# Optimization experiments

Measured on AMD Instinct MI355X. Metric: run time of the kernel, lower is better.

Reference implementation:

```python
import jax, jax.numpy as jnp
import numpy as np

BATCH_SIZE = 4096
DIM = 128
TEMPERATURE = 0.5
EPS = 1e-8


def setup_inputs() -> dict:
    key = jax.random.key(0)
    k1, k2 = jax.random.split(key)
    z_i = jax.random.normal(k1, (BATCH_SIZE, DIM), dtype=jnp.float32)
    z_j = jax.random.normal(k2, (BATCH_SIZE, DIM), dtype=jnp.float32)
    return {"z_i": z_i, "z_j": z_j}


def reference(z_i, z_j):
    B = z_i.shape[0]
    N = 2 * B
    z = jnp.concatenate([z_i, z_j], axis=0)  # [N, D]
    # cosine similarity = matmul of L2-normalized rows (avoids the NxNxD broadcast)
    zn = z / jnp.maximum(jnp.linalg.norm(z, axis=1, keepdims=True), EPS)
    sim = (zn @ zn.T) / TEMPERATURE  # [N, N]
    idx = jnp.arange(N)
    # positive pair: row i pairs with row (i+B) mod N (covers both diag offsets +B and -B)
    pos = sim[idx, (idx + B) % N]  # [N]
    # CE over logits [pos, negatives]; the logit set per row is the full sim row
    # minus the self-similarity (diagonal). Mask diagonal with a large negative.
    neg_inf = jnp.asarray(-1e9, sim.dtype)
    sim_masked = jnp.where(idx[:, None] == idx[None, :], neg_inf, sim)
    lse = jax.nn.logsumexp(sim_masked, axis=1)  # [N]
    # CrossEntropyLoss(reduction='sum') with label 0 (the positive), divided by N
    loss = jnp.sum(lse - pos) / N
    return loss
```

## Files before the change

### kernel.cpp

```cpp
#include <hip/hip_runtime.h>
#include <cstdint>


#define BROWS 4096
#define NROWS 8192
#define ROWB  256
#define CSPL  24
#define CTILES 512
#define BRT   256
#define TILEB 4096

typedef __attribute__((ext_vector_type(8))) __bf16    bf16x8;
typedef __attribute__((ext_vector_type(4))) float     f32x4;
typedef __attribute__((ext_vector_type(4))) uint32_t  u32x4;

#define K1F 2.8853900817779268f
#define LN2F 0.69314718055994531f
#define BC8(x) __builtin_bit_cast(bf16x8, x)

__device__ __forceinline__ uint16_t f2bf(float f) {
    uint32_t u = __builtin_bit_cast(uint32_t, f);
    u = (u + 0x7FFFu + ((u >> 16) & 1u)) >> 16;
    return (uint16_t)u;
}
__device__ __forceinline__ float bf2f(uint16_t b) {
    return __builtin_bit_cast(float, ((uint32_t)b) << 16);
}
__device__ __forceinline__ void gload_lds16(const void* g, void* l) {
    __builtin_amdgcn_global_load_lds(
        (const __attribute__((address_space(1))) void*)g,
        (__attribute__((address_space(3))) void*)l, 16, 0, 0);
}

__global__ __launch_bounds__(256) void k_normalize(
    const float* __restrict__ zi, const float* __restrict__ zj,
    uint16_t* __restrict__ znA, uint16_t* __restrict__ znB)
{
    int tid  = threadIdx.x;
    int lane = tid & 63;
    int wid  = tid >> 6;
    int li   = lane & 7;
    int row  = blockIdx.x * 32 + wid * 8 + (lane >> 3);

    const float* src = (row < BROWS) ? (zi + (size_t)row * 128)
                                     : (zj + (size_t)(row - BROWS) * 128);
    float4 v[4];
    const float4* s4 = (const float4*)(src + li * 16);
#pragma unroll
    for (int c = 0; c < 4; ++c) v[c] = s4[c];

    float ss = 0.f;
#pragma unroll
    for (int c = 0; c < 4; ++c)
        ss += v[c].x*v[c].x + v[c].y*v[c].y + v[c].z*v[c].z + v[c].w*v[c].w;
#pragma unroll
    for (int off = 1; off < 8; off <<= 1) ss += __shfl_xor(ss, off);

    float scale = 1.0f / fmaxf(sqrtf(ss), 1e-8f);

    float e[16];
#pragma unroll
    for (int c = 0; c < 4; ++c) {
        e[c*4+0] = v[c].x * scale; e[c*4+1] = v[c].y * scale;
        e[c*4+2] = v[c].z * scale; e[c*4+3] = v[c].w * scale;
    }
    uint32_t wB[8], wA[8];
#pragma unroll
    for (int q = 0; q < 8; ++q) {
        wB[q] = (uint32_t)f2bf(e[2*q])       | ((uint32_t)f2bf(e[2*q+1])       << 16);
        wA[q] = (uint32_t)f2bf(e[2*q] * K1F) | ((uint32_t)f2bf(e[2*q+1] * K1F) << 16);
    }
    uint4* dB = (uint4*)((char*)znB + (size_t)row * ROWB + li * 32);
    dB[0] = make_uint4(wB[0], wB[1], wB[2], wB[3]);
    dB[1] = make_uint4(wB[4], wB[5], wB[6], wB[7]);
    uint4* dA = (uint4*)((char*)znA + (size_t)row * ROWB + li * 32);
    dA[0] = make_uint4(wA[0], wA[1], wA[2], wA[3]);
    dA[1] = make_uint4(wA[4], wA[5], wA[6], wA[7]);
}

__global__ __launch_bounds__(256)
__attribute__((amdgpu_waves_per_eu(3, 3)))
void k_simlse(
    const uint16_t* __restrict__ znA, const uint16_t* __restrict__ znB,
    float* __restrict__ partial)
{
    __shared__ __align__(16) char lds[2][TILEB];

    const char* zA = (const char*)znA;
    const char* zB = (const char*)znB;
    int tid  = threadIdx.x;
    int lane = tid & 63;
    int wid  = tid >> 6;
    int lo16 = lane & 15;
    int hi4  = lane >> 4;
    int rowBase = blockIdx.x * BRT + wid * 64;

    u32x4 a[4][4];
#pragma unroll
    for (int rt = 0; rt < 4; ++rt) {
        const char* ap = zA + (size_t)(rowBase + rt * 16 + lo16) * ROWB + hi4 * 16;
#pragma unroll
        for (int kf = 0; kf < 4; ++kf)
            a[rt][kf] = *(const u32x4*)(ap + kf * 64);
    }

    float rs[4][4];
#pragma unroll
    for (int rt = 0; rt < 4; ++rt)
#pragma unroll
        for (int r = 0; r < 4; ++r) rs[rt][r] = 0.f;

    int t0 = (CTILES * blockIdx.y) / CSPL;
    int t1 = (CTILES * (blockIdx.y + 1)) / CSPL;
    int nt = t1 - t0;

    const char* gsrc = zB + (size_t)t0 * TILEB
                     + ((tid * 16) ^ (((tid >> 4) & 7) << 4));
    char* ldst[2] = { &lds[0][wid * 1024], &lds[1][wid * 1024] };
    int  xorv = (lo16 & 7) << 4;

#define STAGE(sel, t) gload_lds16(gsrc + (size_t)(t) * TILEB, ldst[sel])

#define COMPUTE(sel) do {                                                        \
        const char* lb_ = &lds[sel][lo16 * 256];                                 \
        u32x4 bf[4];                                                             \
        _Pragma("unroll")                                                        \
        for (int kf = 0; kf < 4; ++kf)                                           \
            bf[kf] = *(const u32x4*)(lb_ + ((hi4 * 16 + kf * 64) ^ xorv));       \
        f32x4 ac0 = {0.f,0.f,0.f,0.f}, ac1 = {0.f,0.f,0.f,0.f};                  \
        f32x4 ac2 = {0.f,0.f,0.f,0.f}, ac3 = {0.f,0.f,0.f,0.f};                  \
        _Pragma("unroll")                                                        \
        for (int kf = 0; kf < 4; ++kf) {                                         \
            bf16x8 bk_ = BC8(bf[kf]);                                            \
            ac0 = __builtin_amdgcn_mfma_f32_16x16x32_bf16(BC8(a[0][kf]), bk_, ac0, 0, 0, 0); \
            ac1 = __builtin_amdgcn_mfma_f32_16x16x32_bf16(BC8(a[1][kf]), bk_, ac1, 0, 0, 0); \
            ac2 = __builtin_amdgcn_mfma_f32_16x16x32_bf16(BC8(a[2][kf]), bk_, ac2, 0, 0, 0); \
            ac3 = __builtin_amdgcn_mfma_f32_16x16x32_bf16(BC8(a[3][kf]), bk_, ac3, 0, 0, 0); \
        }                                                                        \
        _Pragma("unroll")                                                        \
        for (int r = 0; r < 4; ++r) {                                            \
            rs[0][r] += __builtin_amdgcn_exp2f(ac0[r]);                          \
            rs[1][r] += __builtin_amdgcn_exp2f(ac1[r]);                          \
            rs[2][r] += __builtin_amdgcn_exp2f(ac2[r]);                          \
            rs[3][r] += __builtin_amdgcn_exp2f(ac3[r]);                          \
        }                                                                        \
    } while (0)

    STAGE(0, 0);
    __syncthreads();

    for (int t = 0; t < nt; ++t) {
        if (t + 1 < nt) STAGE((t + 1) & 1, t + 1);
        COMPUTE(t & 1);
        __syncthreads();
    }

#undef STAGE
#undef COMPUTE

#pragma unroll
    for (int rt = 0; rt < 4; ++rt)
#pragma unroll
        for (int r = 0; r < 4; ++r) {
            float s = rs[rt][r];
            s += __shfl_xor(s, 1);  s += __shfl_xor(s, 2);
            s += __shfl_xor(s, 4);  s += __shfl_xor(s, 8);
            if (lo16 == 0) {
                int row = rowBase + rt * 16 + hi4 * 4 + r;
                partial[blockIdx.y * NROWS + row] = s;
            }
        }
}

__global__ __launch_bounds__(256) void k_finalize(
    const uint16_t* __restrict__ znA, const uint16_t* __restrict__ znB,
    const float* __restrict__ partial, float* __restrict__ blocksum)
{
    int tid = threadIdx.x;
    int i = blockIdx.x * 256 + tid;

    float S = 0.f;
#pragma unroll
    for (int cs = 0; cs < CSPL; ++cs) S += partial[cs * NROWS + i];

    int j = (i + BROWS) & (NROWS - 1);
    const uint4* rAi = (const uint4*)((const char*)znA + (size_t)i * ROWB);
    const uint4* rBi = (const uint4*)((const char*)znB + (size_t)i * ROWB);
    const uint4* rBj = (const uint4*)((const char*)znB + (size_t)j * ROWB);
    float adot = 0.f;
    float sdot = 0.f;
#pragma unroll
    for (int c = 0; c < 16; ++c) {
        uint4 ua = rAi[c], ub = rBi[c], vb = rBj[c];
        const uint32_t* pa = (const uint32_t*)&ua;
        const uint32_t* pb = (const uint32_t*)&ub;
        const uint32_t* pv = (const uint32_t*)&vb;
#pragma unroll
        for (int q = 0; q < 4; ++q) {
            float a0 = bf2f((uint16_t)(pa[q] & 0xffffu)), a1 = bf2f((uint16_t)(pa[q] >> 16));
            float b0 = bf2f((uint16_t)(pb[q] & 0xffffu)), b1 = bf2f((uint16_t)(pb[q] >> 16));
            float v0 = bf2f((uint16_t)(pv[q] & 0xffffu)), v1 = bf2f((uint16_t)(pv[q] >> 16));
            adot += a0 * v0 + a1 * v1;
            sdot += a0 * b0 + a1 * b1;
        }
    }
    S -= __builtin_amdgcn_exp2f(sdot);
    float c = LN2F * (__builtin_amdgcn_logf(S) - adot);

#pragma unroll
    for (int off = 1; off < 64; off <<= 1) c += __shfl_xor(c, off);
    __shared__ float wsum[4];
    int lane = tid & 63, wid = tid >> 6;
    if (lane == 0) wsum[wid] = c;
    __syncthreads();
    if (tid == 0) blocksum[blockIdx.x] = wsum[0] + wsum[1] + wsum[2] + wsum[3];
}

__global__ __launch_bounds__(64) void k_reduce(
    const float* __restrict__ blocksum, float* __restrict__ out)
{
    int tid = threadIdx.x;
    float v = (tid < 32) ? blocksum[tid] : 0.f;
#pragma unroll
    for (int off = 1; off < 64; off <<= 1) v += __shfl_xor(v, off);
    if (tid == 0) out[0] = v * (1.0f / (float)NROWS);
}

extern "C" void kernel_launch(void* const* d_in, const int* in_sizes, int n_in,
                              void* d_out, int out_size, void* d_ws, size_t ws_size,
                              hipStream_t stream)
{
    const float* zi = (const float*)d_in[0];
    const float* zj = (const float*)d_in[1];
    float* out = (float*)d_out;

    char* ws = (char*)d_ws;
    uint16_t* znA      = (uint16_t*)ws;
    uint16_t* znB      = (uint16_t*)(ws + (size_t)NROWS * ROWB);
    float*    partial  = (float*)(ws + 2 * (size_t)NROWS * ROWB);
    float*    blocksum = (float*)(ws + 2 * (size_t)NROWS * ROWB
                                     + (size_t)CSPL * NROWS * 4);

    k_normalize<<<dim3(256), dim3(256), 0, stream>>>(zi, zj, znA, znB);
    k_simlse  <<<dim3(32, CSPL), dim3(256), 0, stream>>>(znA, znB, partial);
    k_finalize<<<dim3(32), dim3(256), 0, stream>>>(znA, znB, partial, blocksum);
    k_reduce  <<<dim3(1), dim3(64), 0, stream>>>(blocksum, out);
}
```

Measured before the change: 41.62 us.

## Triple-buffer 32-column B tiles with prefetch depth two and one barrier

The column tile is doubled to 32 rows of B per stage and the LDS ring grows to three buffers. Loads are now issued two tiles ahead, and explicit vmcnt waits replace the per-iteration __syncthreads, leaving a single s_barrier per tile. The aim is to hide global-to-LDS latency better and to halve the number of loop iterations and barriers. In exchange the block uses three times the LDS (24 KB), which could limit occupancy, and correctness now depends on the hand-written waitcnt counts.

```diff
diff --git a/kernel.cpp b/kernel.cpp
--- a/kernel.cpp
+++ b/kernel.cpp
@@ -6,9 +6,9 @@
 #define NROWS 8192
 #define ROWB  256
 #define CSPL  24
-#define CTILES 512
+#define CT32  256
 #define BRT   256
-#define TILEB 4096
+#define TILEB 8192
 
 typedef __attribute__((ext_vector_type(8))) __bf16    bf16x8;
 typedef __attribute__((ext_vector_type(4))) float     f32x4;
@@ -84,7 +84,7 @@
     const uint16_t* __restrict__ znA, const uint16_t* __restrict__ znB,
     float* __restrict__ partial)
 {
-    __shared__ __align__(16) char lds[2][TILEB];
+    __shared__ __align__(16) char lds[3][TILEB];
 
     const char* zA = (const char*)znA;
     const char* zB = (const char*)znB;
@@ -110,50 +110,63 @@
 #pragma unroll
         for (int r = 0; r < 4; ++r) rs[rt][r] = 0.f;
 
-    int t0 = (CTILES * blockIdx.y) / CSPL;
-    int t1 = (CTILES * (blockIdx.y + 1)) / CSPL;
+    int t0 = (CT32 * blockIdx.y) / CSPL;
+    int t1 = (CT32 * (blockIdx.y + 1)) / CSPL;
     int nt = t1 - t0;
 
     const char* gsrc = zB + (size_t)t0 * TILEB
                      + ((tid * 16) ^ (((tid >> 4) & 7) << 4));
-    char* ldst[2] = { &lds[0][wid * 1024], &lds[1][wid * 1024] };
-    int  xorv = (lo16 & 7) << 4;
-
-#define STAGE(sel, t) gload_lds16(gsrc + (size_t)(t) * TILEB, ldst[sel])
+    int xorv = (lo16 & 7) << 4;
+
+#define STAGE(sel, t) do {                                                     \
+        const char* g_ = gsrc + (size_t)(t) * TILEB;                           \
+        gload_lds16(g_,        &lds[sel][wid * 1024]);                         \
+        gload_lds16(g_ + 4096, &lds[sel][4096 + wid * 1024]);                  \
+    } while (0)
 
 #define COMPUTE(sel) do {                                                        \
-        const char* lb_ = &lds[sel][lo16 * 256];                                 \
-        u32x4 bf[4];                                                             \
         _Pragma("unroll")                                                        \
-        for (int kf = 0; kf < 4; ++kf)                                           \
-            bf[kf] = *(const u32x4*)(lb_ + ((hi4 * 16 + kf * 64) ^ xorv));       \
-        f32x4 ac0 = {0.f,0.f,0.f,0.f}, ac1 = {0.f,0.f,0.f,0.f};                  \
-        f32x4 ac2 = {0.f,0.f,0.f,0.f}, ac3 = {0.f,0.f,0.f,0.f};                  \
-        _Pragma("unroll")                                                        \
-        for (int kf = 0; kf < 4; ++kf) {                                         \
-            bf16x8 bk_ = BC8(bf[kf]);                                            \
-            ac0 = __builtin_amdgcn_mfma_f32_16x16x32_bf16(BC8(a[0][kf]), bk_, ac0, 0, 0, 0); \
-            ac1 = __builtin_amdgcn_mfma_f32_16x16x32_bf16(BC8(a[1][kf]), bk_, ac1, 0, 0, 0); \
-            ac2 = __builtin_amdgcn_mfma_f32_16x16x32_bf16(BC8(a[2][kf]), bk_, ac2, 0, 0, 0); \
-            ac3 = __builtin_amdgcn_mfma_f32_16x16x32_bf16(BC8(a[3][kf]), bk_, ac3, 0, 0, 0); \
-        }                                                                        \
-        _Pragma("unroll")                                                        \
-        for (int r = 0; r < 4; ++r) {                                            \
-            rs[0][r] += __builtin_amdgcn_exp2f(ac0[r]);                          \
-            rs[1][r] += __builtin_amdgcn_exp2f(ac1[r]);                          \
-            rs[2][r] += __builtin_amdgcn_exp2f(ac2[r]);                          \
-            rs[3][r] += __builtin_amdgcn_exp2f(ac3[r]);                          \
+        for (int ct = 0; ct < 2; ++ct) {                                         \
+            const char* lb_ = &lds[sel][ct * 4096 + lo16 * 256];                 \
+            u32x4 bf[4];                                                         \
+            _Pragma("unroll")                                                    \
+            for (int kf = 0; kf < 4; ++kf)                                       \
+                bf[kf] = *(const u32x4*)(lb_ + ((hi4 * 16 + kf * 64) ^ xorv));   \
+            f32x4 ac0 = {0.f,0.f,0.f,0.f}, ac1 = {0.f,0.f,0.f,0.f};              \
+            f32x4 ac2 = {0.f,0.f,0.f,0.f}, ac3 = {0.f,0.f,0.f,0.f};              \
+            _Pragma("unroll")                                                    \
+            for (int kf = 0; kf < 4; ++kf) {                                     \
+                bf16x8 bk_ = BC8(bf[kf]);                                        \
+                ac0 = __builtin_amdgcn_mfma_f32_16x16x32_bf16(BC8(a[0][kf]), bk_, ac0, 0, 0, 0); \
+                ac1 = __builtin_amdgcn_mfma_f32_16x16x32_bf16(BC8(a[1][kf]), bk_, ac1, 0, 0, 0); \
+                ac2 = __builtin_amdgcn_mfma_f32_16x16x32_bf16(BC8(a[2][kf]), bk_, ac2, 0, 0, 0); \
+                ac3 = __builtin_amdgcn_mfma_f32_16x16x32_bf16(BC8(a[3][kf]), bk_, ac3, 0, 0, 0); \
+            }                                                                    \
+            _Pragma("unroll")                                                    \
+            for (int r = 0; r < 4; ++r) {                                        \
+                rs[0][r] += __builtin_amdgcn_exp2f(ac0[r]);                      \
+                rs[1][r] += __builtin_amdgcn_exp2f(ac1[r]);                      \
+                rs[2][r] += __builtin_amdgcn_exp2f(ac2[r]);                      \
+                rs[3][r] += __builtin_amdgcn_exp2f(ac3[r]);                      \
+            }                                                                    \
         }                                                                        \
     } while (0)
 
     STAGE(0, 0);
-    __syncthreads();
-
-    for (int t = 0; t < nt; ++t) {
-        if (t + 1 < nt) STAGE((t + 1) & 1, t + 1);
-        COMPUTE(t & 1);
-        __syncthreads();
-    }
+    STAGE(1, 1);
+
+    int t = 0;
+    for (; t < nt - 1; ++t) {
+        asm volatile("s_waitcnt vmcnt(2)" ::: "memory");
+        __builtin_amdgcn_s_barrier();
+        __builtin_amdgcn_sched_barrier(0);
+        COMPUTE(t % 3);
+        if (t + 2 < nt) STAGE((t + 2) % 3, t + 2);
+    }
+    asm volatile("s_waitcnt vmcnt(0)" ::: "memory");
+    __builtin_amdgcn_s_barrier();
+    __builtin_amdgcn_sched_barrier(0);
+    COMPUTE(t % 3);
 
 #undef STAGE
 #undef COMPUTE
```

Result: faster. 39.09 us (-6.1%).

## Exploit similarity-matrix symmetry by computing only upper-triangular block tiles

Applied to the files above, without the earlier changes.

The similarity kernel now launches one block per half of each upper-triangular 256x256 block pair, using a triangular index mapping. Each tile's exp values feed both the row sums and column sums, and the column sums are written as extra partial slots for the mirrored rows. This roughly halves the MFMA and exp work. It also replaces the double-buffered loop with a fully unrolled four-stage prefetch that uses explicit vmcnt waits. In exchange, finalize reads a variable number of partial slots per row, the workspace for partials grows, and the kernel uses more LDS plus an extra cross-wave column reduction.

```diff
diff --git a/kernel.cpp b/kernel.cpp
--- a/kernel.cpp
+++ b/kernel.cpp
@@ -5,10 +5,8 @@
 #define BROWS 4096
 #define NROWS 8192
 #define ROWB  256
-#define CSPL  24
-#define CTILES 512
-#define BRT   256
-#define TILEB 4096
+#define TILEB 8192
+#define NSLOT 96
 
 typedef __attribute__((ext_vector_type(8))) __bf16    bf16x8;
 typedef __attribute__((ext_vector_type(4))) float     f32x4;
@@ -84,7 +82,8 @@
     const uint16_t* __restrict__ znA, const uint16_t* __restrict__ znB,
     float* __restrict__ partial)
 {
-    __shared__ __align__(16) char lds[2][TILEB];
+    __shared__ __align__(16) char lds[4][TILEB];
+    __shared__ float cslds[4 * 128];
 
     const char* zA = (const char*)znA;
     const char* zB = (const char*)znB;
@@ -93,7 +92,15 @@
     int wid  = tid >> 6;
     int lo16 = lane & 15;
     int hi4  = lane >> 4;
-    int rowBase = blockIdx.x * BRT + wid * 64;
+
+    int q = blockIdx.x;
+    int p = q >> 1, h = q & 1;
+    int s = p / 33, w = p % 33;
+    int bx, by;
+    if (w < 32 - s) { by = s;      bx = s + w; }
+    else            { by = 31 - s; bx = by + (w - (32 - s)); }
+
+    int rowBase = bx * 256 + wid * 64;
 
     u32x4 a[4][4];
 #pragma unroll
@@ -109,67 +116,100 @@
     for (int rt = 0; rt < 4; ++rt)
 #pragma unroll
         for (int r = 0; r < 4; ++r) rs[rt][r] = 0.f;
-
-    int t0 = (CTILES * blockIdx.y) / CSPL;
-    int t1 = (CTILES * (blockIdx.y + 1)) / CSPL;
-    int nt = t1 - t0;
-
-    const char* gsrc = zB + (size_t)t0 * TILEB
+    float cs[8];
+#pragma unroll
+    for (int tg = 0; tg < 8; ++tg) cs[tg] = 0.f;
+
+    const char* gsrc = zB + (size_t)(by * 8 + h * 4) * TILEB
                      + ((tid * 16) ^ (((tid >> 4) & 7) << 4));
-    char* ldst[2] = { &lds[0][wid * 1024], &lds[1][wid * 1024] };
-    int  xorv = (lo16 & 7) << 4;
-
-#define STAGE(sel, t) gload_lds16(gsrc + (size_t)(t) * TILEB, ldst[sel])
-
-#define COMPUTE(sel) do {                                                        \
-        const char* lb_ = &lds[sel][lo16 * 256];                                 \
-        u32x4 bf[4];                                                             \
-        _Pragma("unroll")                                                        \
-        for (int kf = 0; kf < 4; ++kf)                                           \
-            bf[kf] = *(const u32x4*)(lb_ + ((hi4 * 16 + kf * 64) ^ xorv));       \
-        f32x4 ac0 = {0.f,0.f,0.f,0.f}, ac1 = {0.f,0.f,0.f,0.f};                  \
-        f32x4 ac2 = {0.f,0.f,0.f,0.f}, ac3 = {0.f,0.f,0.f,0.f};                  \
-        _Pragma("unroll")                                                        \
-        for (int kf = 0; kf < 4; ++kf) {                                         \
-            bf16x8 bk_ = BC8(bf[kf]);                                            \
-            ac0 = __builtin_amdgcn_mfma_f32_16x16x32_bf16(BC8(a[0][kf]), bk_, ac0, 0, 0, 0); \
-            ac1 = __builtin_amdgcn_mfma_f32_16x16x32_bf16(BC8(a[1][kf]), bk_, ac1, 0, 0, 0); \
-            ac2 = __builtin_amdgcn_mfma_f32_16x16x32_bf16(BC8(a[2][kf]), bk_, ac2, 0, 0, 0); \
-            ac3 = __builtin_amdgcn_mfma_f32_16x16x32_bf16(BC8(a[3][kf]), bk_, ac3, 0, 0, 0); \
-        }                                                                        \
-        _Pragma("unroll")                                                        \
-        for (int r = 0; r < 4; ++r) {                                            \
-            rs[0][r] += __builtin_amdgcn_exp2f(ac0[r]);                          \
-            rs[1][r] += __builtin_amdgcn_exp2f(ac1[r]);                          \
-            rs[2][r] += __builtin_amdgcn_exp2f(ac2[r]);                          \
-            rs[3][r] += __builtin_amdgcn_exp2f(ac3[r]);                          \
-        }                                                                        \
+    int xorv = (lo16 & 7) << 4;
+
+#define STAGE(sel) do {                                                        \
+        const char* g_ = gsrc + (size_t)(sel) * TILEB;                         \
+        gload_lds16(g_,        &lds[sel][wid * 1024]);                         \
+        gload_lds16(g_ + 4096, &lds[sel][4096 + wid * 1024]);                  \
     } while (0)
 
-    STAGE(0, 0);
-    __syncthreads();
-
-    for (int t = 0; t < nt; ++t) {
-        if (t + 1 < nt) STAGE((t + 1) & 1, t + 1);
-        COMPUTE(t & 1);
-        __syncthreads();
-    }
+#define SUBTILE(sel, ct, TG) do {                                              \
+        const char* lb_ = &lds[sel][(ct) * 4096 + lo16 * 256];                 \
+        u32x4 bf0 = *(const u32x4*)(lb_ + ((hi4 * 16 +   0) ^ xorv));          \
+        u32x4 bf1 = *(const u32x4*)(lb_ + ((hi4 * 16 +  64) ^ xorv));          \
+        u32x4 bf2 = *(const u32x4*)(lb_ + ((hi4 * 16 + 128) ^ xorv));          \
+        u32x4 bf3 = *(const u32x4*)(lb_ + ((hi4 * 16 + 192) ^ xorv));          \
+        f32x4 A0 = {0.f,0.f,0.f,0.f}, A1 = {0.f,0.f,0.f,0.f};                  \
+        f32x4 A2 = {0.f,0.f,0.f,0.f}, A3 = {0.f,0.f,0.f,0.f};                  \
+        A0 = __builtin_amdgcn_mfma_f32_16x16x32_bf16(BC8(a[0][0]), BC8(bf0), A0, 0, 0, 0); \
+        A1 = __builtin_amdgcn_mfma_f32_16x16x32_bf16(BC8(a[1][0]), BC8(bf0), A1, 0, 0, 0); \
+        A2 = __builtin_amdgcn_mfma_f32_16x16x32_bf16(BC8(a[2][0]), BC8(bf0), A2, 0, 0, 0); \
+        A3 = __builtin_amdgcn_mfma_f32_16x16x32_bf16(BC8(a[3][0]), BC8(bf0), A3, 0, 0, 0); \
+        A0 = __builtin_amdgcn_mfma_f32_16x16x32_bf16(BC8(a[0][1]), BC8(bf1), A0, 0, 0, 0); \
+        A1 = __builtin_amdgcn_mfma_f32_16x16x32_bf16(BC8(a[1][1]), BC8(bf1), A1, 0, 0, 0); \
+        A2 = __builtin_amdgcn_mfma_f32_16x16x32_bf16(BC8(a[2][1]), BC8(bf1), A2, 0, 0, 0); \
+        A3 = __builtin_amdgcn_mfma_f32_16x16x32_bf16(BC8(a[3][1]), BC8(bf1), A3, 0, 0, 0); \
+        A0 = __builtin_amdgcn_mfma_f32_16x16x32_bf16(BC8(a[0][2]), BC8(bf2), A0, 0, 0, 0); \
+        A1 = __builtin_amdgcn_mfma_f32_16x16x32_bf16(BC8(a[1][2]), BC8(bf2), A1, 0, 0, 0); \
+        A2 = __builtin_amdgcn_mfma_f32_16x16x32_bf16(BC8(a[2][2]), BC8(bf2), A2, 0, 0, 0); \
+        A3 = __builtin_amdgcn_mfma_f32_16x16x32_bf16(BC8(a[3][2]), BC8(bf2), A3, 0, 0, 0); \
+        A0 = __builtin_amdgcn_mfma_f32_16x16x32_bf16(BC8(a[0][3]), BC8(bf3), A0, 0, 0, 0); \
+        A1 = __builtin_amdgcn_mfma_f32_16x16x32_bf16(BC8(a[1][3]), BC8(bf3), A1, 0, 0, 0); \
+        A2 = __builtin_amdgcn_mfma_f32_16x16x32_bf16(BC8(a[2][3]), BC8(bf3), A2, 0, 0, 0); \
+        A3 = __builtin_amdgcn_mfma_f32_16x16x32_bf16(BC8(a[3][3]), BC8(bf3), A3, 0, 0, 0); \
+        float cst = 0.f;                                                       \
+        _Pragma("unroll")                                                      \
+        for (int r = 0; r < 4; ++r) {                                          \
+            float e0 = __builtin_amdgcn_exp2f(A0[r]); rs[0][r] += e0;          \
+            float e1 = __builtin_amdgcn_exp2f(A1[r]); rs[1][r] += e1;          \
+            float e2 = __builtin_amdgcn_exp2f(A2[r]); rs[2][r] += e2;          \
+            float e3 = __builtin_amdgcn_exp2f(A3[r]); rs[3][r] += e3;          \
+            cst += (e0 + e1) + (e2 + e3);                                      \
+        }                                                                      \
+        cs[TG] += cst;                                                         \
+    } while (0)
+
+#define WAITBAR(n) do {                                                       \
+        asm volatile("s_waitcnt vmcnt(" #n ")" ::: "memory");                  \
+        __builtin_amdgcn_s_barrier();                                          \
+        __builtin_amdgcn_sched_barrier(0);                                     \
+    } while (0)
+
+    STAGE(0); STAGE(1); STAGE(2);
+    WAITBAR(4); SUBTILE(0, 0, 0); SUBTILE(0, 1, 1); STAGE(3);
+    WAITBAR(4); SUBTILE(1, 0, 2); SUBTILE(1, 1, 3);
+    WAITBAR(2); SUBTILE(2, 0, 4); SUBTILE(2, 1, 5);
+    WAITBAR(0); SUBTILE(3, 0, 6); SUBTILE(3, 1, 7);
 
 #undef STAGE
-#undef COMPUTE
+#undef SUBTILE
+#undef WAITBAR
 
 #pragma unroll
     for (int rt = 0; rt < 4; ++rt)
 #pragma unroll
         for (int r = 0; r < 4; ++r) {
-            float s = rs[rt][r];
-            s += __shfl_xor(s, 1);  s += __shfl_xor(s, 2);
-            s += __shfl_xor(s, 4);  s += __shfl_xor(s, 8);
+            float v = rs[rt][r];
+            v += __shfl_xor(v, 1);  v += __shfl_xor(v, 2);
+            v += __shfl_xor(v, 4);  v += __shfl_xor(v, 8);
             if (lo16 == 0) {
                 int row = rowBase + rt * 16 + hi4 * 4 + r;
-                partial[blockIdx.y * NROWS + row] = s;
+                partial[(size_t)(2 * by + h) * NROWS + row] = v;
             }
         }
+
+    if (bx != by) {
+#pragma unroll
+        for (int tg = 0; tg < 8; ++tg) {
+            float v = cs[tg];
+            v += __shfl_xor(v, 16);
+            v += __shfl_xor(v, 32);
+            if (hi4 == 0) cslds[wid * 128 + tg * 16 + lo16] = v;
+        }
+        __syncthreads();
+        if (tid < 128) {
+            float v = (cslds[tid] + cslds[128 + tid])
+                    + (cslds[256 + tid] + cslds[384 + tid]);
+            partial[(size_t)(64 + bx) * NROWS + by * 256 + h * 128 + tid] = v;
+        }
+    }
 }
 
 __global__ __launch_bounds__(256) void k_finalize(
@@ -177,11 +217,14 @@
     const float* __restrict__ partial, float* __restrict__ blocksum)
 {
     int tid = threadIdx.x;
-    int i = blockIdx.x * 256 + tid;
+    int R = blockIdx.x;
+    int i = R * 256 + tid;
 
     float S = 0.f;
-#pragma unroll
-    for (int cs = 0; cs < CSPL; ++cs) S += partial[cs * NROWS + i];
+    for (int s2 = 0; s2 < 2 * (R + 1); ++s2)
+        S += partial[(size_t)s2 * NROWS + i];
+    for (int b = R + 1; b < 32; ++b)
+        S += partial[(size_t)(64 + b) * NROWS + i];
 
     int j = (i + BROWS) & (NROWS - 1);
     const uint4* rAi = (const uint4*)((const char*)znA + (size_t)i * ROWB);
@@ -196,10 +239,10 @@
         const uint32_t* pb = (const uint32_t*)&ub;
         const uint32_t* pv = (const uint32_t*)&vb;
 #pragma unroll
-        for (int q = 0; q < 4; ++q) {
-            float a0 = bf2f((uint16_t)(pa[q] & 0xffffu)), a1 = bf2f((uint16_t)(pa[q] >> 16));
-            float b0 = bf2f((uint16_t)(pb[q] & 0xffffu)), b1 = bf2f((uint16_t)(pb[q] >> 16));
-            float v0 = bf2f((uint16_t)(pv[q] & 0xffffu)), v1 = bf2f((uint16_t)(pv[q] >> 16));
+        for (int qq = 0; qq < 4; ++qq) {
+            float a0 = bf2f((uint16_t)(pa[qq] & 0xffffu)), a1 = bf2f((uint16_t)(pa[qq] >> 16));
+            float b0 = bf2f((uint16_t)(pb[qq] & 0xffffu)), b1 = bf2f((uint16_t)(pb[qq] >> 16));
+            float v0 = bf2f((uint16_t)(pv[qq] & 0xffffu)), v1 = bf2f((uint16_t)(pv[qq] >> 16));
             adot += a0 * v0 + a1 * v1;
             sdot += a0 * b0 + a1 * b1;
         }
@@ -239,10 +282,10 @@
     uint16_t* znB      = (uint16_t*)(ws + (size_t)NROWS * ROWB);
     float*    partial  = (float*)(ws + 2 * (size_t)NROWS * ROWB);
     float*    blocksum = (float*)(ws + 2 * (size_t)NROWS * ROWB
-                                     + (size_t)CSPL * NROWS * 4);
+                                     + (size_t)NSLOT * NROWS * 4);
 
     k_normalize<<<dim3(256), dim3(256), 0, stream>>>(zi, zj, znA, znB);
-    k_simlse  <<<dim3(32, CSPL), dim3(256), 0, stream>>>(znA, znB, partial);
+    k_simlse  <<<dim3(1056), dim3(256), 0, stream>>>(znA, znB, partial);
     k_finalize<<<dim3(32), dim3(256), 0, stream>>>(znA, znB, partial, blocksum);
     k_reduce  <<<dim3(1), dim3(64), 0, stream>>>(blocksum, out);
 }
```

Result: slower. 64.76 us (+55.6%).

## Use 64-column tiles with triple-buffered LDS and vmcnt-based waits

Applied to the files above, without the earlier changes.

Each staged tile grows from 16 to 64 B-rows, and LDS goes from double to triple buffering. Loads are issued two tiles ahead, and waits use explicit s_waitcnt vmcnt counts plus a raw barrier, so fewer block-wide barriers are paid per unit of work. The cost is 48KB of LDS per block, which may limit occupancy. Coarser tiles also make the column split less even, since 128 tiles are divided over 24 splits, and the handling of the last two tiles assumes nt >= 2.

```diff
diff --git a/kernel.cpp b/kernel.cpp
--- a/kernel.cpp
+++ b/kernel.cpp
@@ -6,9 +6,9 @@
 #define NROWS 8192
 #define ROWB  256
 #define CSPL  24
-#define CTILES 512
+#define CT64  128
 #define BRT   256
-#define TILEB 4096
+#define TILEB 16384
 
 typedef __attribute__((ext_vector_type(8))) __bf16    bf16x8;
 typedef __attribute__((ext_vector_type(4))) float     f32x4;
@@ -84,7 +84,7 @@
     const uint16_t* __restrict__ znA, const uint16_t* __restrict__ znB,
     float* __restrict__ partial)
 {
-    __shared__ __align__(16) char lds[2][TILEB];
+    __shared__ __align__(16) char lds[3][TILEB];
 
     const char* zA = (const char*)znA;
     const char* zB = (const char*)znB;
@@ -110,63 +110,93 @@
 #pragma unroll
         for (int r = 0; r < 4; ++r) rs[rt][r] = 0.f;
 
-    int t0 = (CTILES * blockIdx.y) / CSPL;
-    int t1 = (CTILES * (blockIdx.y + 1)) / CSPL;
+    int t0 = (CT64 * blockIdx.y) / CSPL;
+    int t1 = (CT64 * (blockIdx.y + 1)) / CSPL;
     int nt = t1 - t0;
 
-    const char* gsrc = zB + (size_t)t0 * TILEB
-                     + ((tid * 16) ^ (((tid >> 4) & 7) << 4));
-    char* ldst[2] = { &lds[0][wid * 1024], &lds[1][wid * 1024] };
-    int  xorv = (lo16 & 7) << 4;
-
-#define STAGE(sel, t) gload_lds16(gsrc + (size_t)(t) * TILEB, ldst[sel])
-
-#define COMPUTE(sel) do {                                                        \
-        const char* lb_ = &lds[sel][lo16 * 256];                                 \
-        u32x4 bf[4];                                                             \
-        _Pragma("unroll")                                                        \
-        for (int kf = 0; kf < 4; ++kf)                                           \
-            bf[kf] = *(const u32x4*)(lb_ + ((hi4 * 16 + kf * 64) ^ xorv));       \
-        f32x4 ac0 = {0.f,0.f,0.f,0.f}, ac1 = {0.f,0.f,0.f,0.f};                  \
-        f32x4 ac2 = {0.f,0.f,0.f,0.f}, ac3 = {0.f,0.f,0.f,0.f};                  \
-        _Pragma("unroll")                                                        \
-        for (int kf = 0; kf < 4; ++kf) {                                         \
-            bf16x8 bk_ = BC8(bf[kf]);                                            \
-            ac0 = __builtin_amdgcn_mfma_f32_16x16x32_bf16(BC8(a[0][kf]), bk_, ac0, 0, 0, 0); \
-            ac1 = __builtin_amdgcn_mfma_f32_16x16x32_bf16(BC8(a[1][kf]), bk_, ac1, 0, 0, 0); \
-            ac2 = __builtin_amdgcn_mfma_f32_16x16x32_bf16(BC8(a[2][kf]), bk_, ac2, 0, 0, 0); \
-            ac3 = __builtin_amdgcn_mfma_f32_16x16x32_bf16(BC8(a[3][kf]), bk_, ac3, 0, 0, 0); \
-        }                                                                        \
-        _Pragma("unroll")                                                        \
-        for (int r = 0; r < 4; ++r) {                                            \
-            rs[0][r] += __builtin_amdgcn_exp2f(ac0[r]);                          \
-            rs[1][r] += __builtin_amdgcn_exp2f(ac1[r]);                          \
-            rs[2][r] += __builtin_amdgcn_exp2f(ac2[r]);                          \
-            rs[3][r] += __builtin_amdgcn_exp2f(ac3[r]);                          \
-        }                                                                        \
-    } while (0)
-
-    STAGE(0, 0);
-    __syncthreads();
-
-    for (int t = 0; t < nt; ++t) {
-        if (t + 1 < nt) STAGE((t + 1) & 1, t + 1);
-        COMPUTE(t & 1);
-        __syncthreads();
-    }
+    const char* gsrc = zB + ((tid * 16) ^ (((tid >> 4) & 7) << 4));
+    int xorv = (lo16 & 7) << 4;
+
+#define STAGE(sel, tt) do {                                                    \
+        const char* g_ = gsrc + (size_t)(tt) * TILEB;                          \
+        char* l_ = &lds[sel][wid * 1024];                                      \
+        gload_lds16(g_,         l_);                                           \
+        gload_lds16(g_ +  4096, l_ +  4096);                                   \
+        gload_lds16(g_ +  8192, l_ +  8192);                                   \
+        gload_lds16(g_ + 12288, l_ + 12288);                                   \
+    } while (0)
+
+#define SUBTILE(sel, ct) do {                                                  \
+        const char* lb_ = &lds[sel][(ct) * 4096 + lo16 * 256];                 \
+        u32x4 bf0 = *(const u32x4*)(lb_ + ((hi4 * 16 +   0) ^ xorv));          \
+        u32x4 bf1 = *(const u32x4*)(lb_ + ((hi4 * 16 +  64) ^ xorv));          \
+        u32x4 bf2 = *(const u32x4*)(lb_ + ((hi4 * 16 + 128) ^ xorv));          \
+        u32x4 bf3 = *(const u32x4*)(lb_ + ((hi4 * 16 + 192) ^ xorv));          \
+        f32x4 A0 = {0.f,0.f,0.f,0.f}, A1 = {0.f,0.f,0.f,0.f};                  \
+        f32x4 A2 = {0.f,0.f,0.f,0.f}, A3 = {0.f,0.f,0.f,0.f};                  \
+        A0 = __builtin_amdgcn_mfma_f32_16x16x32_bf16(BC8(a[0][0]), BC8(bf0), A0, 0, 0, 0); \
+        A1 = __builtin_amdgcn_mfma_f32_16x16x32_bf16(BC8(a[1][0]), BC8(bf0), A1, 0, 0, 0); \
+        A2 = __builtin_amdgcn_mfma_f32_16x16x32_bf16(BC8(a[2][0]), BC8(bf0), A2, 0, 0, 0); \
+        A3 = __builtin_amdgcn_mfma_f32_16x16x32_bf16(BC8(a[3][0]), BC8(bf0), A3, 0, 0, 0); \
+        A0 = __builtin_amdgcn_mfma_f32_16x16x32_bf16(BC8(a[0][1]), BC8(bf1), A0, 0, 0, 0); \
+        A1 = __builtin_amdgcn_mfma_f32_16x16x32_bf16(BC8(a[1][1]), BC8(bf1), A1, 0, 0, 0); \
+        A2 = __builtin_amdgcn_mfma_f32_16x16x32_bf16(BC8(a[2][1]), BC8(bf1), A2, 0, 0, 0); \
+        A3 = __builtin_amdgcn_mfma_f32_16x16x32_bf16(BC8(a[3][1]), BC8(bf1), A3, 0, 0, 0); \
+        A0 = __builtin_amdgcn_mfma_f32_16x16x32_bf16(BC8(a[0][2]), BC8(bf2), A0, 0, 0, 0); \
+        A1 = __builtin_amdgcn_mfma_f32_16x16x32_bf16(BC8(a[1][2]), BC8(bf2), A1, 0, 0, 0); \
+        A2 = __builtin_amdgcn_mfma_f32_16x16x32_bf16(BC8(a[2][2]), BC8(bf2), A2, 0, 0, 0); \
+        A3 = __builtin_amdgcn_mfma_f32_16x16x32_bf16(BC8(a[3][2]), BC8(bf2), A3, 0, 0, 0); \
+        A0 = __builtin_amdgcn_mfma_f32_16x16x32_bf16(BC8(a[0][3]), BC8(bf3), A0, 0, 0, 0); \
+        A1 = __builtin_amdgcn_mfma_f32_16x16x32_bf16(BC8(a[1][3]), BC8(bf3), A1, 0, 0, 0); \
+        A2 = __builtin_amdgcn_mfma_f32_16x16x32_bf16(BC8(a[2][3]), BC8(bf3), A2, 0, 0, 0); \
+        A3 = __builtin_amdgcn_mfma_f32_16x16x32_bf16(BC8(a[3][3]), BC8(bf3), A3, 0, 0, 0); \
+        _Pragma("unroll")                                                      \
+        for (int r = 0; r < 4; ++r) {                                          \
+            rs[0][r] += __builtin_amdgcn_exp2f(A0[r]);                         \
+            rs[1][r] += __builtin_amdgcn_exp2f(A1[r]);                         \
+            rs[2][r] += __builtin_amdgcn_exp2f(A2[r]);                         \
+            rs[3][r] += __builtin_amdgcn_exp2f(A3[r]);                         \
+        }                                                                      \
+    } while (0)
+
+#define COMPUTE(sel) do {                                                      \
+        SUBTILE(sel, 0); SUBTILE(sel, 1);                                      \
+        SUBTILE(sel, 2); SUBTILE(sel, 3);                                      \
+    } while (0)
+
+#define WAITBAR(n) do {                                                       \
+        asm volatile("s_waitcnt vmcnt(" #n ")" ::: "memory");                  \
+        __builtin_amdgcn_s_barrier();                                          \
+        __builtin_amdgcn_sched_barrier(0);                                     \
+    } while (0)
+
+    STAGE(0, t0); STAGE(1, t0 + 1);
+
+    int r = 0;
+    for (; r < nt - 2; ++r) {
+        WAITBAR(4);
+        STAGE((r + 2) % 3, t0 + r + 2);
+        COMPUTE(r % 3);
+    }
+    WAITBAR(4);
+    COMPUTE((nt - 2) % 3);
+    WAITBAR(0);
+    COMPUTE((nt - 1) % 3);
 
 #undef STAGE
+#undef SUBTILE
 #undef COMPUTE
+#undef WAITBAR
 
 #pragma unroll
     for (int rt = 0; rt < 4; ++rt)
 #pragma unroll
-        for (int r = 0; r < 4; ++r) {
-            float s = rs[rt][r];
+        for (int r2 = 0; r2 < 4; ++r2) {
+            float s = rs[rt][r2];
             s += __shfl_xor(s, 1);  s += __shfl_xor(s, 2);
             s += __shfl_xor(s, 4);  s += __shfl_xor(s, 8);
             if (lo16 == 0) {
-                int row = rowBase + rt * 16 + hi4 * 4 + r;
+                int row = rowBase + rt * 16 + hi4 * 4 + r2;
                 partial[blockIdx.y * NROWS + row] = s;
             }
         }
```

After: 49.65 us. +19.3%, slower.
